# Performance work log

Hardware: AMD Instinct MI355X
Metric: run time of the kernel (lower is better)

Reference implementation:

```python
import jax, jax.numpy as jnp
import numpy as np

EPS = 1e-6


def _row_normalize(x):
    return x / (jnp.linalg.norm(x, axis=1, keepdims=True) + EPS)


def _cluster(data, mu, cluster_temp, num_iter):
    # data: [N, D], mu: [K, D]
    data = _row_normalize(data)
    dist = data @ mu.T  # placeholder; overwritten in loop (num_iter >= 1 always here)
    for _ in range(num_iter):
        mu = _row_normalize(mu)
        dist = data @ mu.T                      # [N, K] skinny matmul
        r = jax.nn.softmax(cluster_temp * dist, axis=1)
        cluster_r = r.sum(axis=0)               # [K]
        cluster_mean = r.T @ data               # [K, D]
        mu = cluster_mean / cluster_r[:, None]  # == diag(1/cluster_r) @ cluster_mean
    r = jax.nn.softmax(cluster_temp * dist, axis=1)
    return mu, r


def setup_inputs() -> dict:
    key = jax.random.key(0)
    k1, k2 = jax.random.split(key)
    N, D, K = 200000, 128, 64
    embeds = jax.random.normal(k1, (N, D), dtype=jnp.float32)
    init = jax.random.uniform(k2, (K, D), dtype=jnp.float32)  # torch.rand(K, nout)
    return {"embeds": embeds, "init": init, "cluster_temp": 30}


def reference(embeds, init, cluster_temp):
    temp = jnp.asarray(cluster_temp, dtype=embeds.dtype)
    mu_init, _ = _cluster(embeds, init, temp, num_iter=10)
    mu, r = _cluster(embeds, jax.lax.stop_gradient(mu_init), temp, num_iter=1)
    return mu, r
```

## Files before the change

### kernel.cpp

```cpp
#include <hip/hip_runtime.h>

#define D 128
#define K 64
#define NROWS 200000
#define RT_ROWS 64
#define NTILES (NROWS / RT_ROWS)
#define TPB 256
#define PSLOT (K * D + K)
#define NBLK_MAX 512

typedef __attribute__((ext_vector_type(8))) short bf16x8;
typedef __attribute__((ext_vector_type(4))) float f32x4;

#define XH 0
#define XL 16384
#define ML 32768
#define RTT 49152
#define RSRED 57344
#define LDS_BYTES 58368

__device__ __forceinline__ int xrow_off(int row, int dim) {
  return (row * 256 + dim * 2) ^ ((row & 7) << 4);
}
__device__ __forceinline__ int rt_off(int c, int row) {
  return (c * 128 + row * 2) ^ ((c & 7) << 4);
}
__device__ __forceinline__ ushort f2bf(float x) {
  uint u = __float_as_uint(x);
  return (ushort)((u + 0x7FFF + ((u >> 16) & 1)) >> 16);
}
__device__ __forceinline__ float bf2f(ushort b) {
  return __uint_as_float(((uint)b) << 16);
}

__device__ __forceinline__ void norm_split_store(const float4* xv, char* smem,
                                                 int off_hi, int off_lo,
                                                 int row, int d0) {
  float ss = 0.f;
#pragma unroll
  for (int i = 0; i < 8; ++i)
    ss += xv[i].x * xv[i].x + xv[i].y * xv[i].y + xv[i].z * xv[i].z + xv[i].w * xv[i].w;
  ss += __shfl_xor(ss, 1);
  ss += __shfl_xor(ss, 2);
  const float inv = 1.f / (sqrtf(ss) + 1e-6f);
#pragma unroll
  for (int jb = 0; jb < 4; ++jb) {
    float f[8] = { xv[2*jb].x, xv[2*jb].y, xv[2*jb].z, xv[2*jb].w,
                   xv[2*jb+1].x, xv[2*jb+1].y, xv[2*jb+1].z, xv[2*jb+1].w };
    uint hp[4], lp[4];
#pragma unroll
    for (int q = 0; q < 4; ++q) {
      float a0 = f[2*q] * inv, a1 = f[2*q+1] * inv;
      ushort h0 = f2bf(a0), h1 = f2bf(a1);
      ushort g0 = f2bf(a0 - bf2f(h0)), g1 = f2bf(a1 - bf2f(h1));
      hp[q] = (uint)h0 | ((uint)h1 << 16);
      lp[q] = (uint)g0 | ((uint)g1 << 16);
    }
    *(uint4*)(smem + off_hi + xrow_off(row, d0 + 8*jb)) = make_uint4(hp[0], hp[1], hp[2], hp[3]);
    *(uint4*)(smem + off_lo + xrow_off(row, d0 + 8*jb)) = make_uint4(lp[0], lp[1], lp[2], lp[3]);
  }
}

__global__ __launch_bounds__(TPB, 2) void pass_kernel(
    const float* __restrict__ data, const float* __restrict__ mu_src,
    const int* __restrict__ temp_p, float* __restrict__ partials,
    float* __restrict__ r_out, const int write_r, const int nblk)
{
  __shared__ __align__(16) char smem[LDS_BYTES];
  const int t = threadIdx.x;
  const int w = t >> 6;
  const int l = t & 63;
  const int lg = l >> 4;
  const int lr = l & 15;
  const float temp = (float)(*temp_p);
  const int row_t = t >> 2, d0s = (t & 3) * 32;

  {
    float4 mv[8];
    const float4* src = (const float4*)(mu_src + row_t * D + d0s);
#pragma unroll
    for (int i = 0; i < 8; ++i) mv[i] = src[i];
    norm_split_store(mv, smem, XH, ML, row_t, d0s);
  }
  __syncthreads();
  bf16x8 muh[4][4];
#pragma unroll
  for (int kc = 0; kc < 4; ++kc)
#pragma unroll
    for (int ns = 0; ns < 4; ++ns)
      muh[kc][ns] = *(const bf16x8*)(smem + XH + xrow_off(16*ns + lr, kc*32 + lg*8));
  __syncthreads();

  f32x4 accm[4][2];
#pragma unroll
  for (int ms = 0; ms < 4; ++ms)
#pragma unroll
    for (int n2 = 0; n2 < 2; ++n2) accm[ms][n2] = (f32x4){0.f, 0.f, 0.f, 0.f};
  float rsum[4] = {0.f, 0.f, 0.f, 0.f};

  int tile = blockIdx.x;
  float4 xr[8];
  if (tile < NTILES) {
    const float4* s = (const float4*)(data + (size_t)(tile * RT_ROWS + row_t) * D + d0s);
#pragma unroll
    for (int i = 0; i < 8; ++i) xr[i] = s[i];
  }

  for (; tile < NTILES; tile += nblk) {
    norm_split_store(xr, smem, XH, XL, row_t, d0s);
    __syncthreads();
    const int nxt = tile + nblk;
    if (nxt < NTILES) {
      const float4* s = (const float4*)(data + (size_t)(nxt * RT_ROWS + row_t) * D + d0s);
#pragma unroll
      for (int i = 0; i < 8; ++i) xr[i] = s[i];
    }

    f32x4 pacc[4];
#pragma unroll
    for (int ns = 0; ns < 4; ++ns) pacc[ns] = (f32x4){0.f, 0.f, 0.f, 0.f};
#pragma unroll
    for (int kc = 0; kc < 4; ++kc) {
      const int doff = kc * 32 + lg * 8;
      bf16x8 ah = *(const bf16x8*)(smem + XH + xrow_off(16*w + lr, doff));
      bf16x8 al = *(const bf16x8*)(smem + XL + xrow_off(16*w + lr, doff));
#pragma unroll
      for (int ns = 0; ns < 4; ++ns) {
        bf16x8 bl = *(const bf16x8*)(smem + ML + xrow_off(16*ns + lr, doff));
        pacc[ns] = __builtin_amdgcn_mfma_f32_16x16x32_bf16(ah, muh[kc][ns], pacc[ns], 0, 0, 0);
        pacc[ns] = __builtin_amdgcn_mfma_f32_16x16x32_bf16(al, muh[kc][ns], pacc[ns], 0, 0, 0);
        pacc[ns] = __builtin_amdgcn_mfma_f32_16x16x32_bf16(ah, bl, pacc[ns], 0, 0, 0);
      }
    }

    float rv[4][4], sinv[4];
#pragma unroll
    for (int j = 0; j < 4; ++j) {
      float sj = 0.f;
#pragma unroll
      for (int ns = 0; ns < 4; ++ns) { rv[ns][j] = __expf(temp * pacc[ns][j]); sj += rv[ns][j]; }
      sj += __shfl_xor(sj, 1); sj += __shfl_xor(sj, 2);
      sj += __shfl_xor(sj, 4); sj += __shfl_xor(sj, 8);
      sinv[j] = 1.f / sj;
    }
#pragma unroll
    for (int ns = 0; ns < 4; ++ns) {
      float r0 = rv[ns][0]*sinv[0], r1 = rv[ns][1]*sinv[1],
            r2 = rv[ns][2]*sinv[2], r3 = rv[ns][3]*sinv[3];
      ushort h0 = f2bf(r0), h1 = f2bf(r1), h2 = f2bf(r2), h3 = f2bf(r3);
      rsum[ns] += (bf2f(h0) + bf2f(h1)) + (bf2f(h2) + bf2f(h3));
      uint p0 = (uint)h0 | ((uint)h1 << 16);
      uint p1 = (uint)h2 | ((uint)h3 << 16);
      *(uint2*)(smem + RTT + rt_off(16*ns + lr, 16*w + lg*4)) = make_uint2(p0, p1);
      if (write_r) {
        const size_t rb = (size_t)tile * RT_ROWS + 16*w + lg*4;
        r_out[(rb + 0) * K + 16*ns + lr] = r0;
        r_out[(rb + 1) * K + 16*ns + lr] = r1;
        r_out[(rb + 2) * K + 16*ns + lr] = r2;
        r_out[(rb + 3) * K + 16*ns + lr] = r3;
      }
    }
    __syncthreads();

#pragma unroll
    for (int kc2 = 0; kc2 < 2; ++kc2) {
      const int k0 = kc2 * 32 + lg * 8;
      bf16x8 af[4];
#pragma unroll
      for (int ms = 0; ms < 4; ++ms)
        af[ms] = *(const bf16x8*)(smem + RTT + rt_off(16*ms + lr, k0));
#pragma unroll
      for (int n2 = 0; n2 < 2; ++n2) {
        const int dim = 32*w + 16*n2 + lr;
        bf16x8 bfv;
#pragma unroll
        for (int j = 0; j < 8; ++j)
          bfv[j] = *(const short*)(smem + XH + xrow_off(k0 + j, dim));
#pragma unroll
        for (int ms = 0; ms < 4; ++ms)
          accm[ms][n2] = __builtin_amdgcn_mfma_f32_16x16x32_bf16(af[ms], bfv, accm[ms][n2], 0, 0, 0);
      }
    }
    __syncthreads();
  }

  float* pm = partials + (size_t)blockIdx.x * PSLOT;
#pragma unroll
  for (int ms = 0; ms < 4; ++ms)
#pragma unroll
    for (int n2 = 0; n2 < 2; ++n2)
#pragma unroll
      for (int j = 0; j < 4; ++j)
        pm[(16*ms + lg*4 + j) * D + 32*w + 16*n2 + lr] = accm[ms][n2][j];
#pragma unroll
  for (int ns = 0; ns < 4; ++ns) {
    rsum[ns] += __shfl_xor(rsum[ns], 16);
    rsum[ns] += __shfl_xor(rsum[ns], 32);
  }
  float* rs = (float*)(smem + RSRED);
  if (lg == 0)
#pragma unroll
    for (int ns = 0; ns < 4; ++ns) rs[w * K + 16*ns + lr] = rsum[ns];
  __syncthreads();
  if (t < K) pm[K*D + t] = (rs[t] + rs[K + t]) + (rs[2*K + t] + rs[3*K + t]);
}

__global__ __launch_bounds__(1024) void reduce_update_kernel(
    const float* __restrict__ partials, float* __restrict__ mu_raw,
    float* __restrict__ mu_out, const int write_mu, const int nblk)
{
  __shared__ float red[1024];
  const int c = blockIdx.x >> 2, dq = (blockIdx.x & 3) * 32;
  const int t = threadIdx.x;

  float rp = 0.f;
  for (int b = t; b < nblk; b += 1024) rp += partials[(size_t)b * PSLOT + K*D + c];
  red[t] = rp; __syncthreads();
  if (t < 512) red[t] += red[t + 512];
  __syncthreads();
  if (t < 256) red[t] += red[t + 256];
  __syncthreads();
  if (t < 128) red[t] += red[t + 128];
  __syncthreads();
  if (t < 64) {
    float x = red[t] + red[t + 64];
    x += __shfl_xor(x, 1);  x += __shfl_xor(x, 2);  x += __shfl_xor(x, 4);
    x += __shfl_xor(x, 8);  x += __shfl_xor(x, 16); x += __shfl_xor(x, 32);
    if (t == 0) red[0] = x;
  }
  __syncthreads();
  const float rs_total = red[0];
  __syncthreads();

  const int dl = t & 31, h = t >> 5;
  float s = 0.f;
  for (int b = h; b < nblk; b += 32) s += partials[(size_t)b * PSLOT + c*D + dq + dl];
  red[t] = s; __syncthreads();
  if (t < 512) red[t] += red[t + 512];
  __syncthreads();
  if (t < 256) red[t] += red[t + 256];
  __syncthreads();
  if (t < 128) red[t] += red[t + 128];
  __syncthreads();
  if (t < 64) red[t] += red[t + 64];
  __syncthreads();
  if (t < 32) {
    const float v = (red[t] + red[t + 32]) / rs_total;
    mu_raw[c*D + dq + t] = v;
    if (write_mu) mu_out[c*D + dq + t] = v;
  }
}

extern "C" void kernel_launch(void* const* d_in, const int* in_sizes, int n_in,
                              void* d_out, int out_size, void* d_ws, size_t ws_size,
                              hipStream_t stream)
{
  const float* data = (const float*)d_in[0];
  const float* init = (const float*)d_in[1];
  const int* temp_p = (const int*)d_in[2];
  float* out = (float*)d_out;

  int nblk = NBLK_MAX;
  const size_t need = ((size_t)nblk * PSLOT + (size_t)K * D) * sizeof(float);
  if (ws_size < need) {
    nblk = (int)((ws_size / sizeof(float) - (size_t)K * D) / PSLOT);
    if (nblk < 1) nblk = 1;
  }
  float* partials = (float*)d_ws;
  float* mu_raw = partials + (size_t)nblk * PSLOT;

  for (int it = 0; it < 11; ++it) {
    const float* mu_src = (it == 0) ? init : mu_raw;
    const int last = (it == 10) ? 1 : 0;
    pass_kernel<<<dim3(nblk), dim3(TPB), 0, stream>>>(
        data, mu_src, temp_p, partials, out + K*D, last, nblk);
    reduce_update_kernel<<<dim3(256), dim3(1024), 0, stream>>>(
        partials, mu_raw, out, last, nblk);
  }
}
```

Before: 602.7 us.

## Precompute normalized bf16 split tiles once and accumulate partials with atomics

Adds a prep kernel that normalizes every data row once and writes hi/lo bf16 splits plus a transposed hi copy as 48KB tiles to workspace. Each of the 11 passes then streams these tiles into LDS with global_load_lds, instead of reloading fp32 data and renormalizing it every pass. The transposed copy replaces the strided scalar LDS gathers in the second matmul with vector reads. The mu low part is now held in registers. The per-iteration reduce kernel is replaced by atomicAdd into a zeroed per-iteration slot plus one small final divide. Each pass reads more bytes than the fp32 input, atomic summation order becomes nondeterministic, and the roughly 150MB workspace requirement is no longer checked.

```diff
diff --git a/kernel.cpp b/kernel.cpp
--- a/kernel.cpp
+++ b/kernel.cpp
@@ -6,21 +6,26 @@
 #define RT_ROWS 64
 #define NTILES (NROWS / RT_ROWS)
 #define TPB 256
-#define PSLOT (K * D + K)
-#define NBLK_MAX 512
+#define NBLK 512
+#define TILE_BYTES 49152
+#define PSLOT2 8320
+#define NIT 11
 
 typedef __attribute__((ext_vector_type(8))) short bf16x8;
 typedef __attribute__((ext_vector_type(4))) float f32x4;
 
-#define XH 0
-#define XL 16384
-#define ML 32768
+#define XH  0
+#define XL  16384
+#define XTO 32768
 #define RTT 49152
-#define RSRED 57344
+#define RSO 57344
 #define LDS_BYTES 58368
 
 __device__ __forceinline__ int xrow_off(int row, int dim) {
   return (row * 256 + dim * 2) ^ ((row & 7) << 4);
+}
+__device__ __forceinline__ int xt_off(int dim, int row) {
+  return (dim * 128 + row * 2) ^ ((dim & 7) << 4);
 }
 __device__ __forceinline__ int rt_off(int c, int row) {
   return (c * 128 + row * 2) ^ ((c & 7) << 4);
@@ -32,63 +37,113 @@
 __device__ __forceinline__ float bf2f(ushort b) {
   return __uint_as_float(((uint)b) << 16);
 }
-
-__device__ __forceinline__ void norm_split_store(const float4* xv, char* smem,
-                                                 int off_hi, int off_lo,
-                                                 int row, int d0) {
+__device__ __forceinline__ float dot4(const float4 a, const float4 b) {
+  return a.x * b.x + a.y * b.y + a.z * b.z + a.w * b.w;
+}
+__device__ __forceinline__ void gload16(const char* g, char* l) {
+  __builtin_amdgcn_global_load_lds(
+      (__attribute__((address_space(1))) void*)(g),
+      (__attribute__((address_space(3))) void*)(l), 16, 0, 0);
+}
+
+__global__ __launch_bounds__(TPB) void prep_kernel(
+    const float* __restrict__ data, char* __restrict__ prep)
+{
+  __shared__ __align__(16) char smem[TILE_BYTES];
+  const int t = threadIdx.x;
+  const int tile = blockIdx.x;
+  const int row = t >> 2, d0 = (t & 3) * 32;
+
+  const float4* src = (const float4*)(data + (size_t)(tile * RT_ROWS + row) * D + d0);
+  float xf[32];
   float ss = 0.f;
 #pragma unroll
-  for (int i = 0; i < 8; ++i)
-    ss += xv[i].x * xv[i].x + xv[i].y * xv[i].y + xv[i].z * xv[i].z + xv[i].w * xv[i].w;
+  for (int i = 0; i < 8; ++i) {
+    float4 v = src[i];
+    ss += dot4(v, v);
+    xf[4 * i] = v.x; xf[4 * i + 1] = v.y; xf[4 * i + 2] = v.z; xf[4 * i + 3] = v.w;
+  }
   ss += __shfl_xor(ss, 1);
   ss += __shfl_xor(ss, 2);
   const float inv = 1.f / (sqrtf(ss) + 1e-6f);
-#pragma unroll
-  for (int jb = 0; jb < 4; ++jb) {
-    float f[8] = { xv[2*jb].x, xv[2*jb].y, xv[2*jb].z, xv[2*jb].w,
-                   xv[2*jb+1].x, xv[2*jb+1].y, xv[2*jb+1].z, xv[2*jb+1].w };
+
+  ushort hs[32], ls[32];
+#pragma unroll
+  for (int e = 0; e < 32; ++e) {
+    const float a = xf[e] * inv;
+    const ushort h = f2bf(a);
+    hs[e] = h;
+    ls[e] = f2bf(a - bf2f(h));
+  }
+#pragma unroll
+  for (int j = 0; j < 4; ++j) {
     uint hp[4], lp[4];
 #pragma unroll
     for (int q = 0; q < 4; ++q) {
-      float a0 = f[2*q] * inv, a1 = f[2*q+1] * inv;
-      ushort h0 = f2bf(a0), h1 = f2bf(a1);
-      ushort g0 = f2bf(a0 - bf2f(h0)), g1 = f2bf(a1 - bf2f(h1));
-      hp[q] = (uint)h0 | ((uint)h1 << 16);
-      lp[q] = (uint)g0 | ((uint)g1 << 16);
-    }
-    *(uint4*)(smem + off_hi + xrow_off(row, d0 + 8*jb)) = make_uint4(hp[0], hp[1], hp[2], hp[3]);
-    *(uint4*)(smem + off_lo + xrow_off(row, d0 + 8*jb)) = make_uint4(lp[0], lp[1], lp[2], lp[3]);
-  }
+      hp[q] = (uint)hs[8*j + 2*q] | ((uint)hs[8*j + 2*q + 1] << 16);
+      lp[q] = (uint)ls[8*j + 2*q] | ((uint)ls[8*j + 2*q + 1] << 16);
+    }
+    *(uint4*)(smem + XH + xrow_off(row, d0 + 8*j)) = make_uint4(hp[0], hp[1], hp[2], hp[3]);
+    *(uint4*)(smem + XL + xrow_off(row, d0 + 8*j)) = make_uint4(lp[0], lp[1], lp[2], lp[3]);
+  }
+#pragma unroll
+  for (int e = 0; e < 32; ++e)
+    *(ushort*)(smem + XTO + xt_off(d0 + e, row)) = hs[e];
+  __syncthreads();
+  char* gout = prep + (size_t)tile * TILE_BYTES;
+#pragma unroll
+  for (int i = 0; i < 12; ++i)
+    *(uint4*)(gout + i * 4096 + t * 16) = *(const uint4*)(smem + i * 4096 + t * 16);
 }
 
 __global__ __launch_bounds__(TPB, 2) void pass_kernel(
-    const float* __restrict__ data, const float* __restrict__ mu_src,
-    const int* __restrict__ temp_p, float* __restrict__ partials,
-    float* __restrict__ r_out, const int write_r, const int nblk)
+    const char* __restrict__ prep, const float* __restrict__ mu_src,
+    const int* __restrict__ temp_p, float* __restrict__ acc_slot,
+    float* __restrict__ r_out, const int write_r)
 {
   __shared__ __align__(16) char smem[LDS_BYTES];
   const int t = threadIdx.x;
-  const int w = t >> 6;
-  const int l = t & 63;
-  const int lg = l >> 4;
-  const int lr = l & 15;
+  const int w = t >> 6, l = t & 63, lg = l >> 4, lr = l & 15;
   const float temp = (float)(*temp_p);
-  const int row_t = t >> 2, d0s = (t & 3) * 32;
 
   {
-    float4 mv[8];
-    const float4* src = (const float4*)(mu_src + row_t * D + d0s);
-#pragma unroll
-    for (int i = 0; i < 8; ++i) mv[i] = src[i];
-    norm_split_store(mv, smem, XH, ML, row_t, d0s);
-  }
-  __syncthreads();
-  bf16x8 muh[4][4];
+    const int row = t >> 2, d0 = (t & 3) * 32;
+    const float4* src = (const float4*)(mu_src + row * D + d0);
+    float mf[32];
+    float ss = 0.f;
+#pragma unroll
+    for (int i = 0; i < 8; ++i) {
+      float4 v = src[i];
+      ss += dot4(v, v);
+      mf[4*i] = v.x; mf[4*i+1] = v.y; mf[4*i+2] = v.z; mf[4*i+3] = v.w;
+    }
+    ss += __shfl_xor(ss, 1);
+    ss += __shfl_xor(ss, 2);
+    const float inv = 1.f / (sqrtf(ss) + 1e-6f);
+#pragma unroll
+    for (int j = 0; j < 4; ++j) {
+      uint hp[4], lp[4];
+#pragma unroll
+      for (int q = 0; q < 4; ++q) {
+        const float a0 = mf[8*j + 2*q] * inv, a1 = mf[8*j + 2*q + 1] * inv;
+        const ushort h0 = f2bf(a0), h1 = f2bf(a1);
+        const ushort g0 = f2bf(a0 - bf2f(h0)), g1 = f2bf(a1 - bf2f(h1));
+        hp[q] = (uint)h0 | ((uint)h1 << 16);
+        lp[q] = (uint)g0 | ((uint)g1 << 16);
+      }
+      *(uint4*)(smem + XH + xrow_off(row, d0 + 8*j)) = make_uint4(hp[0], hp[1], hp[2], hp[3]);
+      *(uint4*)(smem + XL + xrow_off(row, d0 + 8*j)) = make_uint4(lp[0], lp[1], lp[2], lp[3]);
+    }
+  }
+  __syncthreads();
+  bf16x8 muh[4][4], mul[4][4];
 #pragma unroll
   for (int kc = 0; kc < 4; ++kc)
 #pragma unroll
-    for (int ns = 0; ns < 4; ++ns)
+    for (int ns = 0; ns < 4; ++ns) {
       muh[kc][ns] = *(const bf16x8*)(smem + XH + xrow_off(16*ns + lr, kc*32 + lg*8));
+      mul[kc][ns] = *(const bf16x8*)(smem + XL + xrow_off(16*ns + lr, kc*32 + lg*8));
+    }
   __syncthreads();
 
   f32x4 accm[4][2];
@@ -98,23 +153,12 @@
     for (int n2 = 0; n2 < 2; ++n2) accm[ms][n2] = (f32x4){0.f, 0.f, 0.f, 0.f};
   float rsum[4] = {0.f, 0.f, 0.f, 0.f};
 
-  int tile = blockIdx.x;
-  float4 xr[8];
-  if (tile < NTILES) {
-    const float4* s = (const float4*)(data + (size_t)(tile * RT_ROWS + row_t) * D + d0s);
-#pragma unroll
-    for (int i = 0; i < 8; ++i) xr[i] = s[i];
-  }
-
-  for (; tile < NTILES; tile += nblk) {
-    norm_split_store(xr, smem, XH, XL, row_t, d0s);
+  for (int tile = blockIdx.x; tile < NTILES; tile += NBLK) {
+    const char* g = prep + (size_t)tile * TILE_BYTES + w * 1024 + l * 16;
+#pragma unroll
+    for (int i = 0; i < 12; ++i)
+      gload16(g + i * 4096, smem + i * 4096 + w * 1024);
     __syncthreads();
-    const int nxt = tile + nblk;
-    if (nxt < NTILES) {
-      const float4* s = (const float4*)(data + (size_t)(nxt * RT_ROWS + row_t) * D + d0s);
-#pragma unroll
-      for (int i = 0; i < 8; ++i) xr[i] = s[i];
-    }
 
     f32x4 pacc[4];
 #pragma unroll
@@ -122,14 +166,13 @@
 #pragma unroll
     for (int kc = 0; kc < 4; ++kc) {
       const int doff = kc * 32 + lg * 8;
-      bf16x8 ah = *(const bf16x8*)(smem + XH + xrow_off(16*w + lr, doff));
-      bf16x8 al = *(const bf16x8*)(smem + XL + xrow_off(16*w + lr, doff));
+      const bf16x8 ah = *(const bf16x8*)(smem + XH + xrow_off(16*w + lr, doff));
+      const bf16x8 al = *(const bf16x8*)(smem + XL + xrow_off(16*w + lr, doff));
 #pragma unroll
       for (int ns = 0; ns < 4; ++ns) {
-        bf16x8 bl = *(const bf16x8*)(smem + ML + xrow_off(16*ns + lr, doff));
         pacc[ns] = __builtin_amdgcn_mfma_f32_16x16x32_bf16(ah, muh[kc][ns], pacc[ns], 0, 0, 0);
         pacc[ns] = __builtin_amdgcn_mfma_f32_16x16x32_bf16(al, muh[kc][ns], pacc[ns], 0, 0, 0);
-        pacc[ns] = __builtin_amdgcn_mfma_f32_16x16x32_bf16(ah, bl, pacc[ns], 0, 0, 0);
+        pacc[ns] = __builtin_amdgcn_mfma_f32_16x16x32_bf16(ah, mul[kc][ns], pacc[ns], 0, 0, 0);
       }
     }
 
@@ -145,13 +188,12 @@
     }
 #pragma unroll
     for (int ns = 0; ns < 4; ++ns) {
-      float r0 = rv[ns][0]*sinv[0], r1 = rv[ns][1]*sinv[1],
-            r2 = rv[ns][2]*sinv[2], r3 = rv[ns][3]*sinv[3];
-      ushort h0 = f2bf(r0), h1 = f2bf(r1), h2 = f2bf(r2), h3 = f2bf(r3);
+      const float r0 = rv[ns][0]*sinv[0], r1 = rv[ns][1]*sinv[1],
+                  r2 = rv[ns][2]*sinv[2], r3 = rv[ns][3]*sinv[3];
+      const ushort h0 = f2bf(r0), h1 = f2bf(r1), h2 = f2bf(r2), h3 = f2bf(r3);
       rsum[ns] += (bf2f(h0) + bf2f(h1)) + (bf2f(h2) + bf2f(h3));
-      uint p0 = (uint)h0 | ((uint)h1 << 16);
-      uint p1 = (uint)h2 | ((uint)h3 << 16);
-      *(uint2*)(smem + RTT + rt_off(16*ns + lr, 16*w + lg*4)) = make_uint2(p0, p1);
+      *(uint2*)(smem + RTT + rt_off(16*ns + lr, 16*w + lg*4)) =
+          make_uint2((uint)h0 | ((uint)h1 << 16), (uint)h2 | ((uint)h3 << 16));
       if (write_r) {
         const size_t rb = (size_t)tile * RT_ROWS + 16*w + lg*4;
         r_out[(rb + 0) * K + 16*ns + lr] = r0;
@@ -172,83 +214,41 @@
 #pragma unroll
       for (int n2 = 0; n2 < 2; ++n2) {
         const int dim = 32*w + 16*n2 + lr;
-        bf16x8 bfv;
-#pragma unroll
-        for (int j = 0; j < 8; ++j)
-          bfv[j] = *(const short*)(smem + XH + xrow_off(k0 + j, dim));
+        const bf16x8 bv = *(const bf16x8*)(smem + XTO + xt_off(dim, k0));
 #pragma unroll
         for (int ms = 0; ms < 4; ++ms)
-          accm[ms][n2] = __builtin_amdgcn_mfma_f32_16x16x32_bf16(af[ms], bfv, accm[ms][n2], 0, 0, 0);
+          accm[ms][n2] = __builtin_amdgcn_mfma_f32_16x16x32_bf16(af[ms], bv, accm[ms][n2], 0, 0, 0);
       }
     }
     __syncthreads();
   }
 
-  float* pm = partials + (size_t)blockIdx.x * PSLOT;
 #pragma unroll
   for (int ms = 0; ms < 4; ++ms)
 #pragma unroll
     for (int n2 = 0; n2 < 2; ++n2)
 #pragma unroll
       for (int j = 0; j < 4; ++j)
-        pm[(16*ms + lg*4 + j) * D + 32*w + 16*n2 + lr] = accm[ms][n2][j];
+        atomicAdd(&acc_slot[(16*ms + lg*4 + j) * D + 32*w + 16*n2 + lr], accm[ms][n2][j]);
 #pragma unroll
   for (int ns = 0; ns < 4; ++ns) {
     rsum[ns] += __shfl_xor(rsum[ns], 16);
     rsum[ns] += __shfl_xor(rsum[ns], 32);
   }
-  float* rs = (float*)(smem + RSRED);
+  float* rs = (float*)(smem + RSO);
   if (lg == 0)
 #pragma unroll
     for (int ns = 0; ns < 4; ++ns) rs[w * K + 16*ns + lr] = rsum[ns];
   __syncthreads();
-  if (t < K) pm[K*D + t] = (rs[t] + rs[K + t]) + (rs[2*K + t] + rs[3*K + t]);
-}
-
-__global__ __launch_bounds__(1024) void reduce_update_kernel(
-    const float* __restrict__ partials, float* __restrict__ mu_raw,
-    float* __restrict__ mu_out, const int write_mu, const int nblk)
-{
-  __shared__ float red[1024];
-  const int c = blockIdx.x >> 2, dq = (blockIdx.x & 3) * 32;
-  const int t = threadIdx.x;
-
-  float rp = 0.f;
-  for (int b = t; b < nblk; b += 1024) rp += partials[(size_t)b * PSLOT + K*D + c];
-  red[t] = rp; __syncthreads();
-  if (t < 512) red[t] += red[t + 512];
-  __syncthreads();
-  if (t < 256) red[t] += red[t + 256];
-  __syncthreads();
-  if (t < 128) red[t] += red[t + 128];
-  __syncthreads();
-  if (t < 64) {
-    float x = red[t] + red[t + 64];
-    x += __shfl_xor(x, 1);  x += __shfl_xor(x, 2);  x += __shfl_xor(x, 4);
-    x += __shfl_xor(x, 8);  x += __shfl_xor(x, 16); x += __shfl_xor(x, 32);
-    if (t == 0) red[0] = x;
-  }
-  __syncthreads();
-  const float rs_total = red[0];
-  __syncthreads();
-
-  const int dl = t & 31, h = t >> 5;
-  float s = 0.f;
-  for (int b = h; b < nblk; b += 32) s += partials[(size_t)b * PSLOT + c*D + dq + dl];
-  red[t] = s; __syncthreads();
-  if (t < 512) red[t] += red[t + 512];
-  __syncthreads();
-  if (t < 256) red[t] += red[t + 256];
-  __syncthreads();
-  if (t < 128) red[t] += red[t + 128];
-  __syncthreads();
-  if (t < 64) red[t] += red[t + 64];
-  __syncthreads();
-  if (t < 32) {
-    const float v = (red[t] + red[t + 32]) / rs_total;
-    mu_raw[c*D + dq + t] = v;
-    if (write_mu) mu_out[c*D + dq + t] = v;
-  }
+  if (t < K)
+    atomicAdd(&acc_slot[K*D + t], (rs[t] + rs[K + t]) + (rs[2*K + t] + rs[3*K + t]));
+}
+
+__global__ __launch_bounds__(TPB) void final_kernel(
+    const float* __restrict__ slot, float* __restrict__ mu_out)
+{
+  const int idx = blockIdx.x * TPB + threadIdx.x;
+  mu_out[idx] = slot[idx] / slot[K * D + (idx >> 7)];
 }
 
 extern "C" void kernel_launch(void* const* d_in, const int* in_sizes, int n_in,
@@ -260,21 +260,17 @@
   const int* temp_p = (const int*)d_in[2];
   float* out = (float*)d_out;
 
-  int nblk = NBLK_MAX;
-  const size_t need = ((size_t)nblk * PSLOT + (size_t)K * D) * sizeof(float);
-  if (ws_size < need) {
-    nblk = (int)((ws_size / sizeof(float) - (size_t)K * D) / PSLOT);
-    if (nblk < 1) nblk = 1;
-  }
-  float* partials = (float*)d_ws;
-  float* mu_raw = partials + (size_t)nblk * PSLOT;
-
-  for (int it = 0; it < 11; ++it) {
-    const float* mu_src = (it == 0) ? init : mu_raw;
-    const int last = (it == 10) ? 1 : 0;
-    pass_kernel<<<dim3(nblk), dim3(TPB), 0, stream>>>(
-        data, mu_src, temp_p, partials, out + K*D, last, nblk);
-    reduce_update_kernel<<<dim3(256), dim3(1024), 0, stream>>>(
-        partials, mu_raw, out, last, nblk);
-  }
-}
+  char* prep = (char*)d_ws;
+  float* slots = (float*)(prep + (size_t)NTILES * TILE_BYTES);
+
+  hipMemsetAsync(slots, 0, (size_t)NIT * PSLOT2 * sizeof(float), stream);
+  prep_kernel<<<dim3(NTILES), dim3(TPB), 0, stream>>>(data, prep);
+
+  for (int it = 0; it < NIT; ++it) {
+    const float* mu_src = (it == 0) ? init : (slots + (size_t)(it - 1) * PSLOT2);
+    pass_kernel<<<dim3(NBLK), dim3(TPB), 0, stream>>>(
+        prep, mu_src, temp_p, slots + (size_t)it * PSLOT2, out + K*D, it == NIT - 1);
+  }
+  final_kernel<<<dim3(32), dim3(TPB), 0, stream>>>(
+      slots + (size_t)(NIT - 1) * PSLOT2, out);
+}
```

After: 702.6 us. +16.6%, slower.
